# Optimization experiments

Hardware: AMD Instinct MI355X
Metric: run time of the kernel (lower is better)

Reference implementation:

```python
import jax, jax.numpy as jnp
import numpy as np

NUM_VIEW, NUM_ANGLE, NUM_DEPTH = 300, 12, 4
GRASP_MAX_WIDTH = 0.1
B, N_SEED, N_GP = 2, 1024, 1024


def _views_np(n=NUM_VIEW):
    # Fibonacci-sphere view sampling (generate_grasp_views)
    phi = (np.sqrt(5.0) - 1.0) / 2.0
    i = np.arange(n, dtype=np.float64)
    z = (2.0 * i + 1.0) / n - 1.0
    r = np.sqrt(np.maximum(1.0 - z * z, 0.0))
    x = r * np.cos(2.0 * np.pi * i * phi)
    y = r * np.sin(2.0 * np.pi * i * phi)
    return np.stack([x, y, z], 1).astype(np.float32)


def _viewpoint_to_matrix(towards, angle):
    # batch_viewpoint_params_to_matrix
    ax = towards / jnp.linalg.norm(towards, axis=1, keepdims=True)
    ay = jnp.stack([-ax[:, 1], ax[:, 0], jnp.zeros_like(ax[:, 0])], 1)
    n = jnp.linalg.norm(ay, axis=1, keepdims=True)
    ay = jnp.where(n > 1e-8, ay / jnp.maximum(n, 1e-12), jnp.array([0.0, 1.0, 0.0], ax.dtype))
    az = jnp.cross(ax, ay)
    R2 = jnp.stack([ax, ay, az], axis=2)  # columns = axes
    c, s = jnp.cos(angle), jnp.sin(angle)
    o, zr = jnp.ones_like(c), jnp.zeros_like(c)
    R1 = jnp.stack([o, zr, zr, zr, c, -s, zr, s, c], 1).reshape(-1, 3, 3)
    return R2 @ R1

VIEWS = jnp.asarray(_views_np())                                   # (V,3)
_ANG = jnp.asarray((np.pi / NUM_ANGLE) * np.arange(NUM_ANGLE, dtype=np.float32))
ANGLES_REP = jnp.tile(_ANG, NUM_VIEW)
VIEWS_REP = jnp.repeat(VIEWS, NUM_ANGLE, axis=0)
GRASP_ROT = _viewpoint_to_matrix(-VIEWS_REP, ANGLES_REP)           # (V*A,3,3)
DEPTHS = jnp.linspace(0.01, 0.04, NUM_DEPTH)
SCORE_BINS = jnp.asarray([0.1, 0.2, 0.3, 0.4, 0.5, 0.6, 0.7, 0.8, 0.9], jnp.float32)
WIDTH_BINS = jnp.asarray([0.02, 0.04, 0.06, 0.08], jnp.float32)
# gripper key points in local frame for width=depth=0.02 (batch_get_key_points)
_LOCAL = jnp.asarray([[0.02, 0.0, 0.0], [0.02, 0.01, 0.0], [0.02, -0.01, 0.0], [0.0, 0.0, 0.0]], jnp.float32)
_LOCAL_SYM = _LOCAL * jnp.asarray([1.0, -1.0, 1.0], jnp.float32)


def _kp12(R, local):
    # rotate the 4 local key points, flatten to 12-dim descriptor
    return jnp.einsum('mij,kj->mki', R, local).reshape(R.shape[0], 12)


def _sqdist(a, b):
    # squared euclidean distances (M,D)x(L,D)->(M,L)
    return jnp.sum(a * a, -1)[:, None] + jnp.sum(b * b, -1)[None, :] - 2.0 * (a @ b.T)


def _rot6d_to_matrix(r6):
    a1, a2 = r6[:, :3], r6[:, 3:]
    b1 = a1 / jnp.linalg.norm(a1, axis=-1, keepdims=True)
    a2p = a2 - jnp.sum(b1 * a2, -1, keepdims=True) * b1
    b2 = a2p / jnp.linalg.norm(a2p, axis=-1, keepdims=True)
    b3 = jnp.cross(b1, b2)
    return jnp.stack([b1, b2, b3], axis=1)  # rows


def _align_angle(rot_trans, scores, widths):
    # align_angle_index: per-view angle matching with 180-deg symmetry
    V, A = NUM_VIEW, NUM_ANGLE
    pkp = _kp12(GRASP_ROT, _LOCAL).reshape(V, A, 12)
    tR = rot_trans.reshape(-1, 3, 3)
    tkp = _kp12(tR, _LOCAL).reshape(V, A, 12)
    tkps = _kp12(tR, _LOCAL_SYM).reshape(V, A, 12)
    d1 = jnp.sum((pkp[:, :, None] - tkp[:, None]) ** 2, -1)   # (V,A,A)
    d2 = jnp.sum((pkp[:, :, None] - tkps[:, None]) ** 2, -1)
    inds = jnp.where(jnp.min(d1, -1) < jnp.min(d2, -1), jnp.argmin(d1, -1), jnp.argmin(d2, -1))  # (V,A)
    rot_out = jnp.take_along_axis(rot_trans, jnp.broadcast_to(inds[:, :, None, None], rot_trans.shape), axis=1)
    idx_s = jnp.broadcast_to(inds[None, :, :, None], scores.shape)
    return rot_out, jnp.take_along_axis(scores, idx_s, 2), jnp.take_along_axis(widths, idx_s, 2)


def _match_one(seed_xyz, pose, gpoints, gscores, gwidths, rot6d, depthp):
    V, A, D = NUM_VIEW, NUM_ANGLE, NUM_DEPTH
    R, t = pose[:, :3], pose[:, 3]
    gp_trans = gpoints @ R.T + t
    views_trans = VIEWS @ R.T
    view_inds = jnp.argmin(_sqdist(VIEWS, views_trans), axis=1)             # (V,)
    rot_trans = jnp.einsum('ij,mjk->mik', R, GRASP_ROT).reshape(V, A, 3, 3)[view_inds]
    gscores = gscores[:, view_inds]
    gwidths = gwidths[:, view_inds]
    rot_trans, gscores, gwidths = _align_angle(rot_trans, gscores, gwidths)
    # nearest GT grasp point for every seed point
    nn = jnp.argmin(_sqdist(seed_xyz, gp_trans), axis=1)                    # (N,)
    gp_sel = gp_trans[nn]
    sc = gscores[nn]                                                        # (N,V,A,D)
    wd = gwidths[nn]
    # keypoint KNN of predicted rotation vs all V*A templates.
    # Pred and template key points share the same seed center and fixed
    # width/depth=0.02, so centers cancel in the distances.
    Rp = _rot6d_to_matrix(rot6d)
    pbase = _kp12(Rp, _LOCAL)                                               # (N,12)
    tR = rot_trans.reshape(-1, 3, 3)
    tbase = _kp12(tR, _LOCAL)                                               # (V*A,12)
    tbase_s = _kp12(tR, _LOCAL_SYM)
    d1 = _sqdist(pbase, tbase)
    d2 = _sqdist(pbase, tbase_s)
    rot_inds = jnp.where(jnp.min(d1, 1) < jnp.min(d2, 1), jnp.argmin(d1, 1), jnp.argmin(d2, 1))  # (N,)
    depth_inds = jnp.argmin(jnp.abs(depthp - DEPTHS[None, :]), axis=1)      # (N,)
    lin = rot_inds * D + depth_inds                                         # ravel_index
    n = seed_xyz.shape[0]
    ar = jnp.arange(n)
    gt_w = wd.reshape(n, -1)[ar, lin][:, None]
    gt_s = sc.reshape(n, -1)[ar, lin][:, None]
    gt_d = DEPTHS[depth_inds][:, None]
    gt_R = tR[rot_inds]
    gt_r6 = gt_R[:, :2, :].reshape(n, 6)                                    # matrix_to_rotation_6d
    return gp_sel, gt_r6, gt_s, gt_w, gt_d


def setup_inputs() -> dict:
    key = jax.random.key(0)
    ks = jax.random.split(key, 6)
    pc = jax.random.normal(ks[0], (B, N_SEED, 3), jnp.float32) * 0.3
    rs = np.random.RandomState(0)
    Rr = np.stack([np.linalg.qr(rs.randn(3, 3))[0] for _ in range(B)]).astype(np.float32)
    det = np.linalg.det(Rr)
    Rr[det < 0, :, 0] *= -1.0
    tt = rs.randn(B, 3, 1).astype(np.float32) * 0.1
    pose = jnp.asarray(np.concatenate([Rr, tt], axis=2))                    # (B,3,4)
    gp = jax.random.normal(ks[1], (B, N_GP, 3), jnp.float32) * 0.05
    labels = jax.random.uniform(ks[2], (B, N_GP, NUM_VIEW, NUM_ANGLE, NUM_DEPTH), jnp.float32)
    offs = jax.random.uniform(ks[3], (B, N_GP, NUM_VIEW, NUM_ANGLE, NUM_DEPTH), jnp.float32) * 0.12
    r6 = jax.random.normal(ks[4], (B, N_SEED, 6), jnp.float32)
    dpred = jax.random.uniform(ks[5], (B, N_SEED, 1), jnp.float32) * 0.05
    return {'point_clouds': pc, 'object_pose': pose, 'grasp_points': gp,
            'grasp_labels': labels, 'grasp_offsets': offs,
            'grasp_rot_pred': r6, 'grasp_depth_pred': dpred}


def reference(point_clouds, object_pose, grasp_points, grasp_labels, grasp_offsets, grasp_rot_pred, grasp_depth_pred):
    pts, rots, sc, wd, dp = jax.vmap(_match_one)(point_clouds, object_pose, grasp_points,
                                                 grasp_labels, grasp_offsets,
                                                 grasp_rot_pred, grasp_depth_pred)
    mask = (sc > 0) & (wd <= GRASP_MAX_WIDTH)
    sc = jnp.where(mask, 1.1 - sc, 0.0)
    width_ids = jnp.searchsorted(WIDTH_BINS, wd)   # torch.bucketize(right=False)
    score_ids = jnp.searchsorted(SCORE_BINS, sc)
    return pts, rots, sc, wd, dp, width_ids, score_ids
```

## Files before the change

### kernel.cpp

```cpp
#include <hip/hip_runtime.h>

#define NV 300
#define NA 12
#define ND 4
#define NM (NV*NA)
#define NS 1024
#define NG 1024

#define W_VIEWS 0
#define W_GROT  900
#define W_PKP   33300
#define W_BATCH 76500
#define SB      134032

#define PB_GPT  0
#define PB_ROT  3072
#define PB_TB   35472
#define PB_TBS  78672
#define PB_TN1  121872
#define PB_TN2  125472
#define PB_VIND 129072
#define PB_AIND 129372
#define PB_NN   132972

__constant__ float C_L[4][3]  = {{0.02f,0.f,0.f},{0.02f,0.01f,0.f},{0.02f,-0.01f,0.f},{0.f,0.f,0.f}};
__constant__ float C_LS[4][3] = {{0.02f,0.f,0.f},{0.02f,-0.01f,0.f},{0.02f,0.01f,0.f},{0.f,0.f,0.f}};

__device__ __forceinline__ void kp12(const float R[9], const float (*L)[3], float out[12]) {
#pragma unroll
    for (int k = 0; k < 4; ++k)
#pragma unroll
        for (int i = 0; i < 3; ++i)
            out[k*3+i] = R[i*3+0]*L[k][0] + R[i*3+1]*L[k][1] + R[i*3+2]*L[k][2];
}

__device__ __forceinline__ void view_d(int i, float* vx, float* vy, float* vz) {
    const double PI = 3.14159265358979323846;
    double phi = (sqrt(5.0) - 1.0) * 0.5;
    double z = (2.0*i + 1.0)/(double)NV - 1.0;
    double r2 = 1.0 - z*z; r2 = r2 > 0.0 ? r2 : 0.0;
    double r = sqrt(r2);
    double ang = 2.0*PI*(double)i*phi;
    *vx = (float)(r*cos(ang));
    *vy = (float)(r*sin(ang));
    *vz = (float)z;
}

__global__ void k_setup(const float* __restrict__ pose, const float* __restrict__ gp,
                        float* W) {
    int bid = blockIdx.x;
    if (bid < 15) {
        int m = bid*256 + threadIdx.x;
        if (m >= NM) return;
        if (m < NV) {
            float x,y,z; view_d(m, &x,&y,&z);
            W[W_VIEWS + 3*m+0] = x; W[W_VIEWS + 3*m+1] = y; W[W_VIEWS + 3*m+2] = z;
        }
        int vi = m / NA, ai = m % NA;
        float vx,vy,vz; view_d(vi, &vx,&vy,&vz);
        float tx = -vx, ty = -vy, tz = -vz;
        float nrm = sqrtf(tx*tx + ty*ty + tz*tz);
        float ax0 = tx/nrm, ax1 = ty/nrm, ax2 = tz/nrm;
        float ay0 = -ax1, ay1 = ax0, ay2 = 0.f;
        float n2 = sqrtf(ay0*ay0 + ay1*ay1 + ay2*ay2);
        if (n2 > 1e-8f) { float d = fmaxf(n2, 1e-12f); ay0 /= d; ay1 /= d; ay2 /= d; }
        else { ay0 = 0.f; ay1 = 1.f; ay2 = 0.f; }
        float az0 = ax1*ay2 - ax2*ay1;
        float az1 = ax2*ay0 - ax0*ay2;
        float az2 = ax0*ay1 - ax1*ay0;
        float angle = (float)(3.14159265358979323846/12.0*(double)ai);
        float c = cosf(angle), s = sinf(angle);
        float G[9];
        G[0]=ax0; G[1]=ay0*c+az0*s; G[2]=-ay0*s+az0*c;
        G[3]=ax1; G[4]=ay1*c+az1*s; G[5]=-ay1*s+az1*c;
        G[6]=ax2; G[7]=ay2*c+az2*s; G[8]=-ay2*s+az2*c;
#pragma unroll
        for (int q=0;q<9;++q) W[W_GROT + 9*m + q] = G[q];
        float pk[12]; kp12(G, C_L, pk);
#pragma unroll
        for (int q=0;q<12;++q) W[W_PKP + 12*m + q] = pk[q];
    } else {
        int idx = (bid-15)*256 + threadIdx.x;
        int b = idx >> 10, g = idx & (NG-1);
        const float* P = pose + 12*b;
        float x = gp[(size_t)idx*3+0], y = gp[(size_t)idx*3+1], z = gp[(size_t)idx*3+2];
        float* o = W + W_BATCH + (size_t)b*SB + PB_GPT + 3*g;
        o[0] = P[0]*x + P[1]*y + P[2]*z  + P[3];
        o[1] = P[4]*x + P[5]*y + P[6]*z  + P[7];
        o[2] = P[8]*x + P[9]*y + P[10]*z + P[11];
    }
}

__global__ void k_va(const float* __restrict__ pose, float* W) {
    int v = blockIdx.x, b = blockIdx.y;
    float* WB = W + W_BATCH + (size_t)b*SB;
    int* IB = (int*)W + W_BATCH + (size_t)b*SB;
    const float* P = pose + 12*b;
    int lane = threadIdx.x;

    __shared__ float vtx[NV], vty[NV], vtz[NV], vn[NV];
    __shared__ float rtr[NA][9];
    __shared__ float tk[NA][12], tks[NA][12];
    __shared__ int s_vi;

    for (int i = lane; i < NV; i += 64) {
        float x = W[W_VIEWS+3*i], y = W[W_VIEWS+3*i+1], z = W[W_VIEWS+3*i+2];
        float a = P[0]*x+P[1]*y+P[2]*z;
        float c = P[4]*x+P[5]*y+P[6]*z;
        float d = P[8]*x+P[9]*y+P[10]*z;
        vtx[i]=a; vty[i]=c; vtz[i]=d;
        vn[i] = a*a + c*c + d*d;
    }
    __syncthreads();
    {
        float x = W[W_VIEWS+3*v], y = W[W_VIEWS+3*v+1], z = W[W_VIEWS+3*v+2];
        float na = x*x + y*y + z*z;
        float best = INFINITY; int bi = 0x7fffffff;
        for (int v2 = lane; v2 < NV; v2 += 64) {
            float d = na + vn[v2] - 2.f*(x*vtx[v2] + y*vty[v2] + z*vtz[v2]);
            if (d < best) { best = d; bi = v2; }
        }
#pragma unroll
        for (int off = 32; off > 0; off >>= 1) {
            float ov = __shfl_down(best, off); int oi = __shfl_down(bi, off);
            if (ov < best || (ov == best && oi < bi)) { best = ov; bi = oi; }
        }
        if (lane == 0) { s_vi = bi; IB[PB_VIND + v] = bi; }
    }
    __syncthreads();
    int vi = s_vi;
    int a = lane;
    if (a < NA) {
        const float* G = W + W_GROT + 9*(vi*NA + a);
        float rt[9];
#pragma unroll
        for (int i=0;i<3;++i)
#pragma unroll
            for (int j=0;j<3;++j)
                rt[i*3+j] = P[i*4+0]*G[0*3+j] + P[i*4+1]*G[1*3+j] + P[i*4+2]*G[2*3+j];
#pragma unroll
        for (int q=0;q<9;++q) rtr[a][q]=rt[q];
        float t1[12], t2[12];
        kp12(rt, C_L, t1); kp12(rt, C_LS, t2);
#pragma unroll
        for (int k=0;k<12;++k) { tk[a][k]=t1[k]; tks[a][k]=t2[k]; }
    }
    __syncthreads();
    if (a < NA) {
        const float* pk = W + W_PKP + 12*(v*NA + a);
        float pkl[12];
#pragma unroll
        for (int k=0;k<12;++k) pkl[k]=pk[k];
        float m1=INFINITY, m2=INFINITY; int i1=0, i2=0;
        for (int ap=0; ap<NA; ++ap) {
            float d1=0.f, d2=0.f;
#pragma unroll
            for (int k=0;k<12;++k) {
                float e1 = pkl[k]-tk[ap][k];  d1 += e1*e1;
                float e2 = pkl[k]-tks[ap][k]; d2 += e2*e2;
            }
            if (d1 < m1) { m1=d1; i1=ap; }
            if (d2 < m2) { m2=d2; i2=ap; }
        }
        int ind = (m1 < m2) ? i1 : i2;
        int mi = v*NA + a;
        IB[PB_AIND + mi] = ind;
        float sel[9];
#pragma unroll
        for (int q=0;q<9;++q) { sel[q]=rtr[ind][q]; WB[PB_ROT + 9*mi + q] = sel[q]; }
        float tb[12], tbs[12];
        kp12(sel, C_L, tb); kp12(sel, C_LS, tbs);
        float s1=0.f, s2=0.f;
#pragma unroll
        for (int k=0;k<12;++k) {
            WB[PB_TB +k*NM+mi]=tb[k];  s1 += tb[k]*tb[k];
            WB[PB_TBS+k*NM+mi]=tbs[k]; s2 += tbs[k]*tbs[k];
        }
        WB[PB_TN1+mi]=s1; WB[PB_TN2+mi]=s2;
    }
}

__global__ void k_nf(const float* __restrict__ pc,
                     const float* __restrict__ r6p, const float* __restrict__ dpp,
                     const float* __restrict__ labels, const float* __restrict__ offsets,
                     float* __restrict__ W, float* __restrict__ out, int B) {
    int b = blockIdx.y;
    int s = blockIdx.x;
    int tid = threadIdx.x;
    int wv = tid >> 6, lane = tid & 63;
    float* WB = W + W_BATCH + (size_t)b*SB;
    const int* IB = (const int*)W + W_BATCH + (size_t)b*SB;

    __shared__ float gx[NG], gy[NG], gz[NG], gn[NG];
    for (int i = tid; i < NG; i += 256) {
        float x = WB[PB_GPT+3*i], y = WB[PB_GPT+3*i+1], z = WB[PB_GPT+3*i+2];
        gx[i]=x; gy[i]=y; gz[i]=z; gn[i]=x*x+y*y+z*z;
    }
    __syncthreads();

    float px = pc[((size_t)b*NS+s)*3+0], py = pc[((size_t)b*NS+s)*3+1], pz = pc[((size_t)b*NS+s)*3+2];
    float pn = px*px+py*py+pz*pz;
    float nbest = INFINITY; int nbi = 0x7fffffff;
    for (int g = tid; g < NG; g += 256) {
        float d = pn + gn[g] - 2.f*(px*gx[g]+py*gy[g]+pz*gz[g]);
        if (d < nbest) { nbest = d; nbi = g; }
    }
#pragma unroll
    for (int off = 32; off > 0; off >>= 1) {
        float ov = __shfl_down(nbest, off); int oi = __shfl_down(nbi, off);
        if (ov < nbest || (ov == nbest && oi < nbi)) { nbest = ov; nbi = oi; }
    }
    __shared__ float snv[4]; __shared__ int sni[4];
    if (lane == 0) { snv[wv] = nbest; sni[wv] = nbi; }

    const float* r6 = r6p + 6*((size_t)b*NS+s);
    float a1x=r6[0],a1y=r6[1],a1z=r6[2],a2x=r6[3],a2y=r6[4],a2z=r6[5];
    float n1 = sqrtf(a1x*a1x+a1y*a1y+a1z*a1z);
    float b1x=a1x/n1, b1y=a1y/n1, b1z=a1z/n1;
    float dt = b1x*a2x+b1y*a2y+b1z*a2z;
    float p2x=a2x-dt*b1x, p2y=a2y-dt*b1y, p2z=a2z-dt*b1z;
    float n2 = sqrtf(p2x*p2x+p2y*p2y+p2z*p2z);
    float b2x=p2x/n2, b2y=p2y/n2, b2z=p2z/n2;
    float b3x=b1y*b2z-b1z*b2y, b3y=b1z*b2x-b1x*b2z, b3z=b1x*b2y-b1y*b2x;
    float Rp[9] = {b1x,b1y,b1z, b2x,b2y,b2z, b3x,b3y,b3z};
    float pb[12]; kp12(Rp, C_L, pb);
    float Pn = 0.f;
#pragma unroll
    for (int k=0;k<12;++k) Pn += pb[k]*pb[k];

    float m1=INFINITY, m2=INFINITY; int i1=0x7fffffff, i2=0x7fffffff;
#pragma unroll
    for (int it = 0; it < 4; ++it) {
        int j0 = it*1024 + tid*4;
        if (j0 < NM) {
            float dot1[4] = {0.f,0.f,0.f,0.f};
            float dot2[4] = {0.f,0.f,0.f,0.f};
#pragma unroll
            for (int k=0;k<12;++k) {
                float4 tb  = *reinterpret_cast<const float4*>(&WB[PB_TB  + k*NM + j0]);
                float4 tbs = *reinterpret_cast<const float4*>(&WB[PB_TBS + k*NM + j0]);
                dot1[0] += pb[k]*tb.x;  dot1[1] += pb[k]*tb.y;
                dot1[2] += pb[k]*tb.z;  dot1[3] += pb[k]*tb.w;
                dot2[0] += pb[k]*tbs.x; dot2[1] += pb[k]*tbs.y;
                dot2[2] += pb[k]*tbs.z; dot2[3] += pb[k]*tbs.w;
            }
            float4 tn1 = *reinterpret_cast<const float4*>(&WB[PB_TN1 + j0]);
            float4 tn2 = *reinterpret_cast<const float4*>(&WB[PB_TN2 + j0]);
            float n1v[4] = {tn1.x,tn1.y,tn1.z,tn1.w};
            float n2v[4] = {tn2.x,tn2.y,tn2.z,tn2.w};
#pragma unroll
            for (int q=0;q<4;++q) {
                float d1 = Pn + n1v[q] - 2.f*dot1[q];
                float d2 = Pn + n2v[q] - 2.f*dot2[q];
                int j = j0 + q;
                if (d1 < m1) { m1=d1; i1=j; }
                if (d2 < m2) { m2=d2; i2=j; }
            }
        }
    }
#pragma unroll
    for (int off = 32; off > 0; off >>= 1) {
        float o1 = __shfl_down(m1, off); int oi1 = __shfl_down(i1, off);
        if (o1 < m1 || (o1 == m1 && oi1 < i1)) { m1 = o1; i1 = oi1; }
        float o2 = __shfl_down(m2, off); int oi2 = __shfl_down(i2, off);
        if (o2 < m2 || (o2 == m2 && oi2 < i2)) { m2 = o2; i2 = oi2; }
    }
    __shared__ float sm1[4], sm2[4];
    __shared__ int   si1[4], si2[4];
    if (lane == 0) { sm1[wv]=m1; si1[wv]=i1; sm2[wv]=m2; si2[wv]=i2; }
    __syncthreads();
    if (tid != 0) return;
#pragma unroll
    for (int w = 1; w < 4; ++w) {
        if (sm1[w] < m1 || (sm1[w] == m1 && si1[w] < i1)) { m1 = sm1[w]; i1 = si1[w]; }
        if (sm2[w] < m2 || (sm2[w] == m2 && si2[w] < i2)) { m2 = sm2[w]; i2 = si2[w]; }
        if (snv[w] < nbest || (snv[w] == nbest && sni[w] < nbi)) { nbest = snv[w]; nbi = sni[w]; }
    }
    int rot_ind = (m1 < m2) ? i1 : i2;
    int nn_s = nbi;

    float dp = dpp[(size_t)b*NS+s];
    float bd = INFINITY; int di = 0;
#pragma unroll
    for (int d = 0; d < ND; ++d) {
        float dv = (float)(0.01 + 0.01*(double)d);
        float ad = fabsf(dp - dv);
        if (ad < bd) { bd = ad; di = d; }
    }

    int v_out = rot_ind / NA;
    int vi = IB[PB_VIND + v_out];
    int ai = IB[PB_AIND + rot_ind];
    size_t lidx = ((((size_t)b*NG+nn_s)*NV + vi)*NA + ai)*ND + di;
    float gs = labels[lidx];
    float gw = offsets[lidx];

    int bs = b*NS + s;
    int oRot = B*NS*3;
    int oSc  = oRot + B*NS*6;
    int oWd  = oSc  + B*NS;
    int oDp  = oWd  + B*NS;
    int oWid = oDp  + B*NS;
    int oSid = oWid + B*NS;

    out[3*bs+0]=gx[nn_s]; out[3*bs+1]=gy[nn_s]; out[3*bs+2]=gz[nn_s];
    const float* Rsel = WB + PB_ROT + 9*rot_ind;
#pragma unroll
    for (int q=0;q<6;++q) out[oRot + 6*bs + q] = Rsel[q];

    bool mask = (gs > 0.f) && (gw <= 0.1f);
    float sc = mask ? (1.1f - gs) : 0.f;
    out[oSc + bs] = sc;
    out[oWd + bs] = gw;
    out[oDp + bs] = (float)(0.01 + 0.01*(double)di);

    int wid = 0;
    wid += (0.02f < gw); wid += (0.04f < gw); wid += (0.06f < gw); wid += (0.08f < gw);
    const float sbins[9] = {0.1f,0.2f,0.3f,0.4f,0.5f,0.6f,0.7f,0.8f,0.9f};
    int sid = 0;
#pragma unroll
    for (int i=0;i<9;++i) sid += (sbins[i] < sc) ? 1 : 0;
    out[oWid + bs] = (float)wid;
    out[oSid + bs] = (float)sid;
}

extern "C" void kernel_launch(void* const* d_in, const int* in_sizes, int n_in,
                              void* d_out, int out_size, void* d_ws, size_t ws_size,
                              hipStream_t stream) {
    const float* pc      = (const float*)d_in[0];
    const float* pose    = (const float*)d_in[1];
    const float* gp      = (const float*)d_in[2];
    const float* labels  = (const float*)d_in[3];
    const float* offsets = (const float*)d_in[4];
    const float* r6      = (const float*)d_in[5];
    const float* dpp     = (const float*)d_in[6];
    float* W   = (float*)d_ws;
    float* out = (float*)d_out;
    int B = in_sizes[1] / 12;

    hipLaunchKernelGGL(k_setup, dim3(15 + B*(NG/256)), dim3(256), 0, stream, pose, gp, W);
    hipLaunchKernelGGL(k_va,    dim3(NV, B), dim3(64), 0, stream, pose, W);
    hipLaunchKernelGGL(k_nf,    dim3(NS, B), dim3(256), 0, stream,
                       pc, r6, dpp, labels, offsets, W, out, B);
}
```

Before: 260.7 us.

## Process four seeds per block to reuse template keypoint loads

Each block of k_nf now handles four seed points instead of one. Every template float4 loaded from global memory is applied to all four seeds' keypoint descriptors, which cuts template memory traffic and per-block setup such as the shared grasp-point fill. The nearest grasp-point search is redistributed so each wavefront handles one seed. The cost is higher register pressure from the four sets of accumulators, and the grid shrinks to a quarter of its former size.

```diff
diff --git a/kernel.cpp b/kernel.cpp
--- a/kernel.cpp
+++ b/kernel.cpp
@@ -6,6 +6,7 @@
 #define NM (NV*NA)
 #define NS 1024
 #define NG 1024
+#define NSP 4
 
 #define W_VIEWS 0
 #define W_GROT  900
@@ -21,7 +22,6 @@
 #define PB_TN2  125472
 #define PB_VIND 129072
 #define PB_AIND 129372
-#define PB_NN   132972
 
 __constant__ float C_L[4][3]  = {{0.02f,0.f,0.f},{0.02f,0.01f,0.f},{0.02f,-0.01f,0.f},{0.f,0.f,0.f}};
 __constant__ float C_LS[4][3] = {{0.02f,0.f,0.f},{0.02f,-0.01f,0.f},{0.02f,0.01f,0.f},{0.f,0.f,0.f}};
@@ -185,7 +185,7 @@
                      const float* __restrict__ labels, const float* __restrict__ offsets,
                      float* __restrict__ W, float* __restrict__ out, int B) {
     int b = blockIdx.y;
-    int s = blockIdx.x;
+    int s0 = blockIdx.x*NSP;
     int tid = threadIdx.x;
     int wv = tid >> 6, lane = tid & 63;
     float* WB = W + W_BATCH + (size_t)b*SB;
@@ -198,51 +198,68 @@
     }
     __syncthreads();
 
-    float px = pc[((size_t)b*NS+s)*3+0], py = pc[((size_t)b*NS+s)*3+1], pz = pc[((size_t)b*NS+s)*3+2];
-    float pn = px*px+py*py+pz*pz;
-    float nbest = INFINITY; int nbi = 0x7fffffff;
-    for (int g = tid; g < NG; g += 256) {
-        float d = pn + gn[g] - 2.f*(px*gx[g]+py*gy[g]+pz*gz[g]);
-        if (d < nbest) { nbest = d; nbi = g; }
-    }
-#pragma unroll
-    for (int off = 32; off > 0; off >>= 1) {
-        float ov = __shfl_down(nbest, off); int oi = __shfl_down(nbi, off);
-        if (ov < nbest || (ov == nbest && oi < nbi)) { nbest = ov; nbi = oi; }
-    }
-    __shared__ float snv[4]; __shared__ int sni[4];
-    if (lane == 0) { snv[wv] = nbest; sni[wv] = nbi; }
-
-    const float* r6 = r6p + 6*((size_t)b*NS+s);
-    float a1x=r6[0],a1y=r6[1],a1z=r6[2],a2x=r6[3],a2y=r6[4],a2z=r6[5];
-    float n1 = sqrtf(a1x*a1x+a1y*a1y+a1z*a1z);
-    float b1x=a1x/n1, b1y=a1y/n1, b1z=a1z/n1;
-    float dt = b1x*a2x+b1y*a2y+b1z*a2z;
-    float p2x=a2x-dt*b1x, p2y=a2y-dt*b1y, p2z=a2z-dt*b1z;
-    float n2 = sqrtf(p2x*p2x+p2y*p2y+p2z*p2z);
-    float b2x=p2x/n2, b2y=p2y/n2, b2z=p2z/n2;
-    float b3x=b1y*b2z-b1z*b2y, b3y=b1z*b2x-b1x*b2z, b3z=b1x*b2y-b1y*b2x;
-    float Rp[9] = {b1x,b1y,b1z, b2x,b2y,b2z, b3x,b3y,b3z};
-    float pb[12]; kp12(Rp, C_L, pb);
-    float Pn = 0.f;
-#pragma unroll
-    for (int k=0;k<12;++k) Pn += pb[k]*pb[k];
-
-    float m1=INFINITY, m2=INFINITY; int i1=0x7fffffff, i2=0x7fffffff;
+    __shared__ int s_nn[NSP];
+    {
+        int s = s0 + wv;
+        float px = pc[((size_t)b*NS+s)*3+0], py = pc[((size_t)b*NS+s)*3+1], pz = pc[((size_t)b*NS+s)*3+2];
+        float pn = px*px+py*py+pz*pz;
+        float nbest = INFINITY; int nbi = 0x7fffffff;
+        for (int g = lane; g < NG; g += 64) {
+            float d = pn + gn[g] - 2.f*(px*gx[g]+py*gy[g]+pz*gz[g]);
+            if (d < nbest) { nbest = d; nbi = g; }
+        }
+#pragma unroll
+        for (int off = 32; off > 0; off >>= 1) {
+            float ov = __shfl_down(nbest, off); int oi = __shfl_down(nbi, off);
+            if (ov < nbest || (ov == nbest && oi < nbi)) { nbest = ov; nbi = oi; }
+        }
+        if (lane == 0) s_nn[wv] = nbi;
+    }
+
+    float pb[NSP][12]; float Pn[NSP];
+#pragma unroll
+    for (int ss = 0; ss < NSP; ++ss) {
+        const float* r6 = r6p + 6*((size_t)b*NS + s0 + ss);
+        float a1x=r6[0],a1y=r6[1],a1z=r6[2],a2x=r6[3],a2y=r6[4],a2z=r6[5];
+        float n1 = sqrtf(a1x*a1x+a1y*a1y+a1z*a1z);
+        float b1x=a1x/n1, b1y=a1y/n1, b1z=a1z/n1;
+        float dt = b1x*a2x+b1y*a2y+b1z*a2z;
+        float p2x=a2x-dt*b1x, p2y=a2y-dt*b1y, p2z=a2z-dt*b1z;
+        float n2 = sqrtf(p2x*p2x+p2y*p2y+p2z*p2z);
+        float b2x=p2x/n2, b2y=p2y/n2, b2z=p2z/n2;
+        float b3x=b1y*b2z-b1z*b2y, b3y=b1z*b2x-b1x*b2z, b3z=b1x*b2y-b1y*b2x;
+        float Rp[9] = {b1x,b1y,b1z, b2x,b2y,b2z, b3x,b3y,b3z};
+        kp12(Rp, C_L, pb[ss]);
+        float pnorm = 0.f;
+#pragma unroll
+        for (int k=0;k<12;++k) pnorm += pb[ss][k]*pb[ss][k];
+        Pn[ss] = pnorm;
+    }
+
+    float m1[NSP], m2[NSP]; int i1[NSP], i2[NSP];
+#pragma unroll
+    for (int ss=0; ss<NSP; ++ss) { m1[ss]=INFINITY; m2[ss]=INFINITY; i1[ss]=0x7fffffff; i2[ss]=0x7fffffff; }
 #pragma unroll
     for (int it = 0; it < 4; ++it) {
         int j0 = it*1024 + tid*4;
         if (j0 < NM) {
-            float dot1[4] = {0.f,0.f,0.f,0.f};
-            float dot2[4] = {0.f,0.f,0.f,0.f};
+            float dot1[NSP][4], dot2[NSP][4];
+#pragma unroll
+            for (int ss=0; ss<NSP; ++ss)
+#pragma unroll
+                for (int q=0;q<4;++q) { dot1[ss][q]=0.f; dot2[ss][q]=0.f; }
 #pragma unroll
             for (int k=0;k<12;++k) {
                 float4 tb  = *reinterpret_cast<const float4*>(&WB[PB_TB  + k*NM + j0]);
                 float4 tbs = *reinterpret_cast<const float4*>(&WB[PB_TBS + k*NM + j0]);
-                dot1[0] += pb[k]*tb.x;  dot1[1] += pb[k]*tb.y;
-                dot1[2] += pb[k]*tb.z;  dot1[3] += pb[k]*tb.w;
-                dot2[0] += pb[k]*tbs.x; dot2[1] += pb[k]*tbs.y;
-                dot2[2] += pb[k]*tbs.z; dot2[3] += pb[k]*tbs.w;
+#pragma unroll
+                for (int ss=0; ss<NSP; ++ss) {
+                    float p = pb[ss][k];
+                    dot1[ss][0] += p*tb.x;  dot1[ss][1] += p*tb.y;
+                    dot1[ss][2] += p*tb.z;  dot1[ss][3] += p*tb.w;
+                    dot2[ss][0] += p*tbs.x; dot2[ss][1] += p*tbs.y;
+                    dot2[ss][2] += p*tbs.z; dot2[ss][3] += p*tbs.w;
+                }
             }
             float4 tn1 = *reinterpret_cast<const float4*>(&WB[PB_TN1 + j0]);
             float4 tn2 = *reinterpret_cast<const float4*>(&WB[PB_TN2 + j0]);
@@ -250,34 +267,49 @@
             float n2v[4] = {tn2.x,tn2.y,tn2.z,tn2.w};
 #pragma unroll
             for (int q=0;q<4;++q) {
-                float d1 = Pn + n1v[q] - 2.f*dot1[q];
-                float d2 = Pn + n2v[q] - 2.f*dot2[q];
                 int j = j0 + q;
-                if (d1 < m1) { m1=d1; i1=j; }
-                if (d2 < m2) { m2=d2; i2=j; }
+#pragma unroll
+                for (int ss=0; ss<NSP; ++ss) {
+                    float d1 = Pn[ss] + n1v[q] - 2.f*dot1[ss][q];
+                    float d2 = Pn[ss] + n2v[q] - 2.f*dot2[ss][q];
+                    if (d1 < m1[ss]) { m1[ss]=d1; i1[ss]=j; }
+                    if (d2 < m2[ss]) { m2[ss]=d2; i2[ss]=j; }
+                }
             }
         }
     }
 #pragma unroll
     for (int off = 32; off > 0; off >>= 1) {
-        float o1 = __shfl_down(m1, off); int oi1 = __shfl_down(i1, off);
-        if (o1 < m1 || (o1 == m1 && oi1 < i1)) { m1 = o1; i1 = oi1; }
-        float o2 = __shfl_down(m2, off); int oi2 = __shfl_down(i2, off);
-        if (o2 < m2 || (o2 == m2 && oi2 < i2)) { m2 = o2; i2 = oi2; }
-    }
-    __shared__ float sm1[4], sm2[4];
-    __shared__ int   si1[4], si2[4];
-    if (lane == 0) { sm1[wv]=m1; si1[wv]=i1; sm2[wv]=m2; si2[wv]=i2; }
-    __syncthreads();
-    if (tid != 0) return;
+#pragma unroll
+        for (int ss=0; ss<NSP; ++ss) {
+            float o1 = __shfl_down(m1[ss], off); int oi1 = __shfl_down(i1[ss], off);
+            if (o1 < m1[ss] || (o1 == m1[ss] && oi1 < i1[ss])) { m1[ss] = o1; i1[ss] = oi1; }
+            float o2 = __shfl_down(m2[ss], off); int oi2 = __shfl_down(i2[ss], off);
+            if (o2 < m2[ss] || (o2 == m2[ss] && oi2 < i2[ss])) { m2[ss] = o2; i2[ss] = oi2; }
+        }
+    }
+    __shared__ float sm1[NSP][4], sm2[NSP][4];
+    __shared__ int   si1[NSP][4], si2[NSP][4];
+    if (lane == 0) {
+#pragma unroll
+        for (int ss=0; ss<NSP; ++ss) {
+            sm1[ss][wv]=m1[ss]; si1[ss][wv]=i1[ss];
+            sm2[ss][wv]=m2[ss]; si2[ss][wv]=i2[ss];
+        }
+    }
+    __syncthreads();
+    if (tid >= NSP) return;
+    int ss = tid;
+    int s = s0 + ss;
+    float M1 = sm1[ss][0], M2 = sm2[ss][0];
+    int   I1 = si1[ss][0], I2 = si2[ss][0];
 #pragma unroll
     for (int w = 1; w < 4; ++w) {
-        if (sm1[w] < m1 || (sm1[w] == m1 && si1[w] < i1)) { m1 = sm1[w]; i1 = si1[w]; }
-        if (sm2[w] < m2 || (sm2[w] == m2 && si2[w] < i2)) { m2 = sm2[w]; i2 = si2[w]; }
-        if (snv[w] < nbest || (snv[w] == nbest && sni[w] < nbi)) { nbest = snv[w]; nbi = sni[w]; }
-    }
-    int rot_ind = (m1 < m2) ? i1 : i2;
-    int nn_s = nbi;
+        if (sm1[ss][w] < M1 || (sm1[ss][w] == M1 && si1[ss][w] < I1)) { M1 = sm1[ss][w]; I1 = si1[ss][w]; }
+        if (sm2[ss][w] < M2 || (sm2[ss][w] == M2 && si2[ss][w] < I2)) { M2 = sm2[ss][w]; I2 = si2[ss][w]; }
+    }
+    int rot_ind = (M1 < M2) ? I1 : I2;
+    int nn_s = s_nn[ss];
 
     float dp = dpp[(size_t)b*NS+s];
     float bd = INFINITY; int di = 0;
@@ -340,6 +372,6 @@
 
     hipLaunchKernelGGL(k_setup, dim3(15 + B*(NG/256)), dim3(256), 0, stream, pose, gp, W);
     hipLaunchKernelGGL(k_va,    dim3(NV, B), dim3(64), 0, stream, pose, W);
-    hipLaunchKernelGGL(k_nf,    dim3(NS, B), dim3(256), 0, stream,
+    hipLaunchKernelGGL(k_nf,    dim3(NS/NSP, B), dim3(256), 0, stream,
                        pc, r6, dpp, labels, offsets, W, out, B);
 }
```

After: 300.8 us. 15.4% more time.
